# Kernel tuning notes

Measured on AMD Instinct MI355X. Metric: run time of the kernel, lower is better.

The kernel has to match this reference:

```python
import jax, jax.numpy as jnp
import numpy as np

# Dimensions derived from Mamba.__init__: d_model=512 -> joint_latent=32, mamb_latent=D=640
NL, D, DIN, DS, DTR, DC = 4, 640, 1280, 16, 40, 4  # n_layer, d_model, d_inner, d_state, dt_rank, d_conv
B, V = 64, 30  # batch, joint-sequence length (repeat_joint_num)


def _rms(x, w, eps=1e-5):
    return x * jax.lax.rsqrt(jnp.mean(x * x, axis=-1, keepdims=True) + eps) * w


def _mamba_block(x, in_w, conv_w, conv_b, xp_w, dt_w, dt_b, A_log, D_skip, out_w):
    # x: [B, V, D]
    u, res = jnp.split(jnp.einsum('bvd,ed->bve', x, in_w), 2, axis=-1)  # each [B,V,DIN]
    # causal depthwise conv1d over V
    xc = jnp.pad(u.transpose(0, 2, 1), ((0, 0), (0, 0), (DC - 1, 0)))  # [B,DIN,V+DC-1]
    xc = jax.lax.conv_general_dilated(xc, conv_w[:, None, :], (1,), 'VALID',
                                      feature_group_count=DIN,
                                      dimension_numbers=('NCH', 'OIH', 'NCH'))
    u = jax.nn.silu(xc.transpose(0, 2, 1) + conv_b)  # [B,V,DIN]
    # input-dependent SSM params
    dbl = jnp.einsum('bvd,ed->bve', u, xp_w)  # [B,V,DTR+2*DS]
    delta, Bm, Cm = jnp.split(dbl, [DTR, DTR + DS], axis=-1)
    delta = jax.nn.softplus(jnp.einsum('bvr,dr->bvd', delta, dt_w) + dt_b)  # [B,V,DIN]
    A = -jnp.exp(A_log)  # [DIN,DS]
    dA = jnp.exp(delta[..., None] * A)                              # [B,V,DIN,DS]
    dBu = delta[..., None] * Bm[:, :, None, :] * u[..., None]       # [B,V,DIN,DS]

    def step(h, t):
        dA_t, dBu_t, C_t = t
        h = dA_t * h + dBu_t                      # [B,DIN,DS]
        return h, jnp.einsum('bds,bs->bd', h, C_t)

    h0 = jnp.zeros((x.shape[0], DIN, DS), x.dtype)
    _, ys = jax.lax.scan(step, h0, (dA.transpose(1, 0, 2, 3),
                                    dBu.transpose(1, 0, 2, 3),
                                    Cm.transpose(1, 0, 2)))
    y = ys.transpose(1, 0, 2) + u * D_skip        # [B,V,DIN]
    return jnp.einsum('bvd,ed->bve', y * jax.nn.silu(res), out_w)


def setup_inputs() -> dict:
    key = jax.random.key(0)
    ks = jax.random.split(key, 10)
    s = 0.02
    return {
        'x': jax.random.normal(ks[0], (B, V, D), jnp.float32),
        'vs': jax.random.randint(ks[1], (B,), 0, V),
        'norm_w': jnp.ones((NL, D), jnp.float32),
        'in_proj_w': s * jax.random.normal(ks[2], (NL, 2 * DIN, D), jnp.float32),
        'conv_w': s * jax.random.normal(ks[3], (NL, DIN, DC), jnp.float32),
        'conv_b': jnp.zeros((NL, DIN), jnp.float32),
        'x_proj_w': s * jax.random.normal(ks[4], (NL, DTR + 2 * DS, DIN), jnp.float32),
        'dt_proj_w': s * jax.random.normal(ks[5], (NL, DIN, DTR), jnp.float32),
        'dt_proj_b': jnp.full((NL, DIN), -4.0, jnp.float32) + 0.1 * jax.random.normal(ks[6], (NL, DIN), jnp.float32),
        'A_log': jnp.tile(jnp.log(jnp.arange(1.0, DS + 1.0, dtype=jnp.float32)), (NL, DIN, 1)),
        'D_skip': jnp.ones((NL, DIN), jnp.float32),
        'out_proj_w': s * jax.random.normal(ks[7], (NL, D, DIN), jnp.float32),
        'norm_f_w': jnp.ones((D,), jnp.float32),
    }


def reference(x, vs, norm_w, in_proj_w, conv_w, conv_b, x_proj_w, dt_proj_w,
              dt_proj_b, A_log, D_skip, out_proj_w, norm_f_w):
    bidx = jnp.arange(x.shape[0])[:, None]
    # batch-wise circular permutation over V (circular_permute_v)
    fwd_idx = (jnp.arange(V)[None, :] + V - vs[:, None]) % V  # [B,V]
    h = x[bidx, fwd_idx]
    for i in range(NL):
        h = h + _mamba_block(_rms(h, norm_w[i]), in_proj_w[i], conv_w[i], conv_b[i],
                             x_proj_w[i], dt_proj_w[i], dt_proj_b[i], A_log[i],
                             D_skip[i], out_proj_w[i])
    h = _rms(h, norm_f_w)
    # reverse_circular_permute_v
    rev_idx = (jnp.arange(V)[None, :] + vs[:, None]) % V
    return h[bidx, rev_idx]
```

## Files before the change

### kernel.cpp

```cpp
#include <hip/hip_runtime.h>
#include <math.h>

#define NLAYER 4
#define DMODEL 640
#define DINNER 1280
#define DSTATE 16
#define DTRANK 40
#define DCONV  4
#define BATCH  64
#define SEQ    30
#define MTOK   (BATCH*SEQ)
#define NPROJ  (2*DINNER)
#define NDBL   (DTRANK+2*DSTATE)
#define NDBLP  80
#define KSEGS  8
#define KSEG   (DINNER/KSEGS)
#define DTKP   64

#define Q1 (NLAYER*NPROJ*DMODEL/4)
#define Q2 (NLAYER*DMODEL*DINNER/4)
#define Q3 (NLAYER*NDBLP*DINNER/4)
#define Q4 (NLAYER*DINNER*DTKP/4)
#define WCTOT (Q1+Q2+Q3+Q4)

typedef unsigned short u16;
typedef __bf16 bf16x8 __attribute__((ext_vector_type(8)));
typedef float  f32x4  __attribute__((ext_vector_type(4)));
typedef unsigned short u16x8 __attribute__((ext_vector_type(8)));

__device__ __forceinline__ float siluf(float x) {
    return x / (1.0f + __expf(-x));
}

__device__ __forceinline__ u16 f2bf(float f) {
    unsigned int u = __float_as_uint(f);
    u += 0x7fffu + ((u >> 16) & 1u);
    return (u16)(u >> 16);
}

__device__ __forceinline__ float bf2f(u16 b) {
    return __uint_as_float(((unsigned int)b) << 16);
}

__global__ void k_permute(const float* __restrict__ x, const int* __restrict__ vs,
                          float* __restrict__ h) {
    int idx = blockIdx.x * blockDim.x + threadIdx.x;
    if (idx >= MTOK * DMODEL) return;
    int d  = idx % DMODEL;
    int mv = idx / DMODEL;
    int v  = mv % SEQ;
    int b  = mv / SEQ;
    int src = (v + SEQ - vs[b]) % SEQ;
    h[idx] = x[(b * SEQ + src) * DMODEL + d];
}

__global__ __launch_bounds__(256)
void k_wconv(const float* __restrict__ in_w, const float* __restrict__ out_w,
             const float* __restrict__ xp_w, const float* __restrict__ dt_w,
             u16* __restrict__ wbi, u16* __restrict__ wbo,
             u16* __restrict__ wbx, u16* __restrict__ wdt) {
    int i = blockIdx.x * 256 + threadIdx.x;
    if (i < Q1) {
        int j = i * 4;
        float4 v = *(const float4*)(in_w + j);
        ushort4 o;
        o.x = f2bf(v.x); o.y = f2bf(v.y); o.z = f2bf(v.z); o.w = f2bf(v.w);
        *(ushort4*)(wbi + j) = o;
    } else if (i < Q1 + Q2) {
        int j = (i - Q1) * 4;
        float4 v = *(const float4*)(out_w + j);
        ushort4 o;
        o.x = f2bf(v.x); o.y = f2bf(v.y); o.z = f2bf(v.z); o.w = f2bf(v.w);
        *(ushort4*)(wbo + j) = o;
    } else if (i < Q1 + Q2 + Q3) {
        int j = (i - Q1 - Q2) * 4;
        int layer = j / (NDBLP * DINNER);
        int rem   = j % (NDBLP * DINNER);
        int r = rem / DINNER, c = rem % DINNER;
        ushort4 o = make_ushort4(0, 0, 0, 0);
        if (r < NDBL) {
            float4 v = *(const float4*)(xp_w + ((size_t)layer * NDBL + r) * DINNER + c);
            o.x = f2bf(v.x); o.y = f2bf(v.y); o.z = f2bf(v.z); o.w = f2bf(v.w);
        }
        *(ushort4*)(wbx + j) = o;
    } else {
        int j = (i - Q1 - Q2 - Q3) * 4;
        int ld = j / DTKP;
        int c  = j % DTKP;
        ushort4 o = make_ushort4(0, 0, 0, 0);
        if (c < DTRANK) {
            float4 v = *(const float4*)(dt_w + (size_t)ld * DTRANK + c);
            o.x = f2bf(v.x); o.y = f2bf(v.y); o.z = f2bf(v.z); o.w = f2bf(v.w);
        }
        *(ushort4*)(wdt + j) = o;
    }
}

__global__ __launch_bounds__(64)
void k_rmsnorm(const float* __restrict__ h, const float* __restrict__ w,
               u16* __restrict__ xn) {
    int m = blockIdx.x;
    int t = threadIdx.x;
    const float* row = h + (size_t)m * DMODEL;
    float2 vv[5];
    float ss = 0.f;
    #pragma unroll
    for (int i = 0; i < 5; ++i) {
        vv[i] = *(const float2*)(row + i * 128 + t * 2);
        ss += vv[i].x * vv[i].x + vv[i].y * vv[i].y;
    }
    #pragma unroll
    for (int o = 32; o > 0; o >>= 1) ss += __shfl_xor(ss, o, 64);
    float sc = rsqrtf(ss / DMODEL + 1e-5f);
    u16* outp = xn + (size_t)m * DMODEL;
    #pragma unroll
    for (int i = 0; i < 5; ++i) {
        int d = i * 128 + t * 2;
        float2 wv = *(const float2*)(w + d);
        ushort2 o;
        o.x = f2bf(vv[i].x * sc * wv.x);
        o.y = f2bf(vv[i].y * sc * wv.y);
        *(ushort2*)(outp + d) = o;
    }
}

__global__ __launch_bounds__(512)
void k_mfma512(const u16* __restrict__ A, int lda,
               const u16* __restrict__ W,
               u16* __restrict__ Cb, int N, int K) {
    __shared__ u16 As[128 * 32];
    __shared__ u16 Bs[128 * 32];
    const int t = threadIdx.x;
    const int w = t >> 6, l = t & 63;
    const int lane15 = l & 15, quad = l >> 4;
    const int wm = w >> 1, wn = w & 1;
    const int m0 = blockIdx.y * 128, n0 = blockIdx.x * 128;

    f32x4 acc[2][4];
    #pragma unroll
    for (int i = 0; i < 2; ++i)
        #pragma unroll
        for (int j = 0; j < 4; ++j)
            acc[i][j] = (f32x4){0.f, 0.f, 0.f, 0.f};

    for (int k0 = 0; k0 < K; k0 += 32) {
        __syncthreads();
        #pragma unroll
        for (int q = 0; q < 2; ++q) {
            int c = q * 512 + t;
            if (c < 512) {
                const u16* ga = A + (size_t)(m0 + (c >> 2)) * lda + k0 + (c & 3) * 8;
                __builtin_amdgcn_global_load_lds(
                    (const __attribute__((address_space(1))) void*)ga,
                    (__attribute__((address_space(3))) void*)&As[c * 8], 16, 0, 0);
            } else {
                int cb = c - 512;
                const u16* gb = W + (size_t)(n0 + (cb >> 2)) * K + k0 + (cb & 3) * 8;
                __builtin_amdgcn_global_load_lds(
                    (const __attribute__((address_space(1))) void*)gb,
                    (__attribute__((address_space(3))) void*)&Bs[cb * 8], 16, 0, 0);
            }
        }
        __syncthreads();

        bf16x8 af[2], bfrag[4];
        #pragma unroll
        for (int i = 0; i < 2; ++i)
            af[i] = *(const bf16x8*)&As[(wm * 32 + i * 16 + lane15) * 32 + quad * 8];
        #pragma unroll
        for (int j = 0; j < 4; ++j)
            bfrag[j] = *(const bf16x8*)&Bs[(wn * 64 + j * 16 + lane15) * 32 + quad * 8];
        #pragma unroll
        for (int i = 0; i < 2; ++i)
            #pragma unroll
            for (int j = 0; j < 4; ++j)
                acc[i][j] = __builtin_amdgcn_mfma_f32_16x16x32_bf16(
                    af[i], bfrag[j], acc[i][j], 0, 0, 0);
    }

    #pragma unroll
    for (int i = 0; i < 2; ++i) {
        #pragma unroll
        for (int r = 0; r < 4; ++r) {
            int row = m0 + wm * 32 + i * 16 + quad * 4 + r;
            #pragma unroll
            for (int j = 0; j < 4; ++j) {
                int col = n0 + wn * 64 + j * 16 + lane15;
                Cb[(size_t)row * N + col] = f2bf(acc[i][j][r]);
            }
        }
    }
}

__global__ __launch_bounds__(256)
void k_mfma64(const u16* __restrict__ A, int lda,
              const u16* __restrict__ W,
              const float* __restrict__ resid,
              float* __restrict__ C, int N, int K) {
    __shared__ u16 As[64 * 32];
    __shared__ u16 Bs[64 * 32];
    const int t = threadIdx.x;
    const int w = t >> 6, l = t & 63;
    const int lane15 = l & 15, quad = l >> 4;
    const int wm = w >> 1, wn = w & 1;
    const int m0 = blockIdx.y * 64, n0 = blockIdx.x * 64;

    f32x4 acc[2][2];
    #pragma unroll
    for (int i = 0; i < 2; ++i)
        #pragma unroll
        for (int j = 0; j < 2; ++j)
            acc[i][j] = (f32x4){0.f, 0.f, 0.f, 0.f};

    for (int k0 = 0; k0 < K; k0 += 32) {
        __syncthreads();
        {
            int c = t;
            const u16* ga = A + (size_t)(m0 + (c >> 2)) * lda + k0 + (c & 3) * 8;
            __builtin_amdgcn_global_load_lds(
                (const __attribute__((address_space(1))) void*)ga,
                (__attribute__((address_space(3))) void*)&As[c * 8], 16, 0, 0);
            const u16* gb = W + (size_t)(n0 + (c >> 2)) * K + k0 + (c & 3) * 8;
            __builtin_amdgcn_global_load_lds(
                (const __attribute__((address_space(1))) void*)gb,
                (__attribute__((address_space(3))) void*)&Bs[c * 8], 16, 0, 0);
        }
        __syncthreads();

        bf16x8 af[2], bfrag[2];
        #pragma unroll
        for (int i = 0; i < 2; ++i)
            af[i] = *(const bf16x8*)&As[(wm * 32 + i * 16 + lane15) * 32 + quad * 8];
        #pragma unroll
        for (int j = 0; j < 2; ++j)
            bfrag[j] = *(const bf16x8*)&Bs[(wn * 32 + j * 16 + lane15) * 32 + quad * 8];
        #pragma unroll
        for (int i = 0; i < 2; ++i)
            #pragma unroll
            for (int j = 0; j < 2; ++j)
                acc[i][j] = __builtin_amdgcn_mfma_f32_16x16x32_bf16(
                    af[i], bfrag[j], acc[i][j], 0, 0, 0);
    }

    #pragma unroll
    for (int i = 0; i < 2; ++i) {
        #pragma unroll
        for (int r = 0; r < 4; ++r) {
            int row = m0 + wm * 32 + i * 16 + quad * 4 + r;
            #pragma unroll
            for (int j = 0; j < 2; ++j) {
                int col = n0 + wn * 32 + j * 16 + lane15;
                size_t idx = (size_t)row * N + col;
                float v = acc[i][j][r];
                if (resid) v += resid[idx];
                C[idx] = v;
            }
        }
    }
}

__global__ __launch_bounds__(256)
void k_conv(const u16* __restrict__ urb, const float* __restrict__ cw,
            const float* __restrict__ cb, u16* __restrict__ ubf) {
    int idx = blockIdx.x * 256 + threadIdx.x;
    int c = idx % DINNER;
    int b = idx / DINNER;
    const u16* up = urb + (size_t)(b * SEQ) * NPROJ + c;
    float xv[SEQ];
    #pragma unroll
    for (int v = 0; v < SEQ; ++v) xv[v] = bf2f(up[(size_t)v * NPROJ]);
    float w0 = cw[c * 4 + 0], w1 = cw[c * 4 + 1];
    float w2 = cw[c * 4 + 2], w3 = cw[c * 4 + 3];
    float bias = cb[c];
    u16* op = ubf + (size_t)(b * SEQ) * DINNER + c;
    float x0 = 0.f, x1 = 0.f, x2 = 0.f;
    #pragma unroll
    for (int v = 0; v < SEQ; ++v) {
        float x3 = xv[v];
        float o = bias + w0 * x0 + w1 * x1 + w2 * x2 + w3 * x3;
        op[(size_t)v * DINNER] = f2bf(siluf(o));
        x0 = x1; x1 = x2; x2 = x3;
    }
}

__global__ __launch_bounds__(256)
void k_xproj(const u16* __restrict__ ubf, const u16* __restrict__ wbx,
             float* __restrict__ dblp) {
    __shared__ u16 As[64 * 32];
    __shared__ u16 Bs[NDBLP * 32];
    const int t = threadIdx.x;
    const int w = t >> 6, l = t & 63;
    const int lane15 = l & 15, quad = l >> 4;
    const int seg = blockIdx.x;
    const int m0 = blockIdx.y * 64;
    const int kb = seg * KSEG;

    f32x4 acc[5];
    #pragma unroll
    for (int j = 0; j < 5; ++j) acc[j] = (f32x4){0.f, 0.f, 0.f, 0.f};

    for (int k0 = 0; k0 < KSEG; k0 += 32) {
        __syncthreads();
        {
            int c = t;
            const u16* ga = ubf + (size_t)(m0 + (c >> 2)) * DINNER + kb + k0 + (c & 3) * 8;
            __builtin_amdgcn_global_load_lds(
                (const __attribute__((address_space(1))) void*)ga,
                (__attribute__((address_space(3))) void*)&As[c * 8], 16, 0, 0);
            const u16* gb = wbx + (size_t)(c >> 2) * DINNER + kb + k0 + (c & 3) * 8;
            __builtin_amdgcn_global_load_lds(
                (const __attribute__((address_space(1))) void*)gb,
                (__attribute__((address_space(3))) void*)&Bs[c * 8], 16, 0, 0);
        }
        if (t < 64) {
            int c = 256 + t;
            const u16* gb = wbx + (size_t)(c >> 2) * DINNER + kb + k0 + (c & 3) * 8;
            __builtin_amdgcn_global_load_lds(
                (const __attribute__((address_space(1))) void*)gb,
                (__attribute__((address_space(3))) void*)&Bs[c * 8], 16, 0, 0);
        }
        __syncthreads();

        bf16x8 af = *(const bf16x8*)&As[(w * 16 + lane15) * 32 + quad * 8];
        #pragma unroll
        for (int j = 0; j < 5; ++j) {
            bf16x8 bfrag = *(const bf16x8*)&Bs[(j * 16 + lane15) * 32 + quad * 8];
            acc[j] = __builtin_amdgcn_mfma_f32_16x16x32_bf16(af, bfrag, acc[j], 0, 0, 0);
        }
    }

    float* outp = dblp + (size_t)seg * MTOK * NDBLP;
    #pragma unroll
    for (int r = 0; r < 4; ++r) {
        int row = m0 + w * 16 + quad * 4 + r;
        #pragma unroll
        for (int j = 0; j < 5; ++j) {
            int col = j * 16 + lane15;
            outp[(size_t)row * NDBLP + col] = acc[j][r];
        }
    }
}

__global__ __launch_bounds__(256)
void k_dtgemm(const float* __restrict__ dblp, const u16* __restrict__ dtwb,
              const float* __restrict__ dtb, u16* __restrict__ delta) {
    __shared__ u16 As[64 * 32];
    __shared__ u16 Bs[64 * 32];
    const int t = threadIdx.x;
    const int w = t >> 6, l = t & 63;
    const int lane15 = l & 15, quad = l >> 4;
    const int wm = w >> 1, wn = w & 1;
    const int m0 = blockIdx.y * 64, n0 = blockIdx.x * 64;
    const int row = t >> 2, koff = (t & 3) * 8;
    const int m = m0 + row;

    f32x4 acc[2][2];
    #pragma unroll
    for (int i = 0; i < 2; ++i)
        #pragma unroll
        for (int j = 0; j < 2; ++j)
            acc[i][j] = (f32x4){0.f, 0.f, 0.f, 0.f};

    #pragma unroll
    for (int k0 = 0; k0 < DTKP; k0 += 32) {
        float sums[8] = {0.f, 0.f, 0.f, 0.f, 0.f, 0.f, 0.f, 0.f};
        #pragma unroll
        for (int q = 0; q < 2; ++q) {
            int col = k0 + koff + q * 4;
            if (col < DTRANK) {
                #pragma unroll
                for (int sg = 0; sg < KSEGS; ++sg) {
                    float4 p = *(const float4*)&dblp[(size_t)sg * MTOK * NDBLP
                                                     + (size_t)m * NDBLP + col];
                    sums[q * 4 + 0] += p.x; sums[q * 4 + 1] += p.y;
                    sums[q * 4 + 2] += p.z; sums[q * 4 + 3] += p.w;
                }
            }
        }
        u16x8 av;
        #pragma unroll
        for (int e = 0; e < 8; ++e) av[e] = f2bf(sums[e]);
        __syncthreads();
        *(u16x8*)&As[row * 32 + koff] = av;
        {
            int c = t;
            const u16* gb = dtwb + (size_t)(n0 + (c >> 2)) * DTKP + k0 + (c & 3) * 8;
            __builtin_amdgcn_global_load_lds(
                (const __attribute__((address_space(1))) void*)gb,
                (__attribute__((address_space(3))) void*)&Bs[c * 8], 16, 0, 0);
        }
        __syncthreads();

        bf16x8 af[2], bfrag[2];
        #pragma unroll
        for (int i = 0; i < 2; ++i)
            af[i] = *(const bf16x8*)&As[(wm * 32 + i * 16 + lane15) * 32 + quad * 8];
        #pragma unroll
        for (int j = 0; j < 2; ++j)
            bfrag[j] = *(const bf16x8*)&Bs[(wn * 32 + j * 16 + lane15) * 32 + quad * 8];
        #pragma unroll
        for (int i = 0; i < 2; ++i)
            #pragma unroll
            for (int j = 0; j < 2; ++j)
                acc[i][j] = __builtin_amdgcn_mfma_f32_16x16x32_bf16(
                    af[i], bfrag[j], acc[i][j], 0, 0, 0);
    }

    #pragma unroll
    for (int i = 0; i < 2; ++i) {
        #pragma unroll
        for (int r = 0; r < 4; ++r) {
            int orow = m0 + wm * 32 + i * 16 + quad * 4 + r;
            #pragma unroll
            for (int j = 0; j < 2; ++j) {
                int col = n0 + wn * 32 + j * 16 + lane15;
                float vv = acc[i][j][r] + dtb[col];
                vv = (vv > 20.f) ? vv : log1pf(__expf(vv));
                delta[(size_t)orow * DINNER + col] = f2bf(vv);
            }
        }
    }
}

__global__ __launch_bounds__(256)
void k_scan(const u16* __restrict__ ubf, const u16* __restrict__ urb,
            const float* __restrict__ dblp, const u16* __restrict__ delta,
            const float* __restrict__ A_log, const float* __restrict__ Dsk,
            u16* __restrict__ y) {
    __shared__ float BC[SEQ][2 * DSTATE];
    const int b  = blockIdx.x / (DINNER / 256);
    const int dc = blockIdx.x % (DINNER / 256);
    const int d  = dc * 256 + threadIdx.x;

    for (int t = threadIdx.x; t < SEQ * 2 * DSTATE; t += 256) {
        int v = t >> 5, s = t & 31;
        float acc = 0.f;
        #pragma unroll
        for (int sg = 0; sg < KSEGS; ++sg)
            acc += dblp[(size_t)sg * MTOK * NDBLP + (size_t)(b * SEQ + v) * NDBLP + DTRANK + s];
        BC[v][s] = acc;
    }
    __syncthreads();

    float dl[SEQ], uu[SEQ], rr[SEQ];
    #pragma unroll
    for (int v = 0; v < SEQ; ++v)
        dl[v] = bf2f(delta[(size_t)(b * SEQ + v) * DINNER + d]);
    #pragma unroll
    for (int v = 0; v < SEQ; ++v)
        uu[v] = bf2f(ubf[(size_t)(b * SEQ + v) * DINNER + d]);
    #pragma unroll
    for (int v = 0; v < SEQ; ++v)
        rr[v] = bf2f(urb[(size_t)(b * SEQ + v) * NPROJ + DINNER + d]);

    float Ar[DSTATE];
    #pragma unroll
    for (int s = 0; s < DSTATE; ++s) Ar[s] = -__expf(A_log[(size_t)d * DSTATE + s]);
    float dsk = Dsk[d];
    float st[DSTATE];
    #pragma unroll
    for (int s = 0; s < DSTATE; ++s) st[s] = 0.f;

    u16* yp = y + (size_t)(b * SEQ) * DINNER + d;

    #pragma unroll
    for (int v = 0; v < SEQ; ++v) {
        float dlt = dl[v];
        float du  = dlt * uu[v];
        float ya0 = 0.f, ya1 = 0.f, ya2 = 0.f, ya3 = 0.f;
        #pragma unroll
        for (int s = 0; s < DSTATE; s += 4) {
            float dA0 = __expf(dlt * Ar[s + 0]);
            float dA1 = __expf(dlt * Ar[s + 1]);
            float dA2 = __expf(dlt * Ar[s + 2]);
            float dA3 = __expf(dlt * Ar[s + 3]);
            st[s + 0] = dA0 * st[s + 0] + du * BC[v][s + 0];
            st[s + 1] = dA1 * st[s + 1] + du * BC[v][s + 1];
            st[s + 2] = dA2 * st[s + 2] + du * BC[v][s + 2];
            st[s + 3] = dA3 * st[s + 3] + du * BC[v][s + 3];
            ya0 += st[s + 0] * BC[v][DSTATE + s + 0];
            ya1 += st[s + 1] * BC[v][DSTATE + s + 1];
            ya2 += st[s + 2] * BC[v][DSTATE + s + 2];
            ya3 += st[s + 3] * BC[v][DSTATE + s + 3];
        }
        float ya = (ya0 + ya1) + (ya2 + ya3);
        yp[(size_t)v * DINNER] = f2bf((ya + uu[v] * dsk) * siluf(rr[v]));
    }
}

__global__ __launch_bounds__(64)
void k_final(const float* __restrict__ h, const int* __restrict__ vs,
             const float* __restrict__ w, float* __restrict__ out) {
    int mv = blockIdx.x;
    int v = mv % SEQ, b = mv / SEQ;
    int src = (v + vs[b]) % SEQ;
    const float* row = h + (size_t)(b * SEQ + src) * DMODEL;
    int t = threadIdx.x;
    float ss = 0.f;
    for (int d = t; d < DMODEL; d += 64) { float x = row[d]; ss += x * x; }
    #pragma unroll
    for (int o = 32; o > 0; o >>= 1) ss += __shfl_xor(ss, o, 64);
    float sc = rsqrtf(ss / DMODEL + 1e-5f);
    float* op = out + (size_t)mv * DMODEL;
    for (int d = t; d < DMODEL; d += 64) op[d] = row[d] * sc * w[d];
}

extern "C" void kernel_launch(void* const* d_in, const int* in_sizes, int n_in,
                              void* d_out, int out_size, void* d_ws, size_t ws_size,
                              hipStream_t stream) {
    const float* x      = (const float*)d_in[0];
    const int*   vs     = (const int*)d_in[1];
    const float* norm_w = (const float*)d_in[2];
    const float* in_w   = (const float*)d_in[3];
    const float* conv_w = (const float*)d_in[4];
    const float* conv_b = (const float*)d_in[5];
    const float* xp_w   = (const float*)d_in[6];
    const float* dt_w   = (const float*)d_in[7];
    const float* dt_b   = (const float*)d_in[8];
    const float* A_log  = (const float*)d_in[9];
    const float* Dsk    = (const float*)d_in[10];
    const float* out_w  = (const float*)d_in[11];
    const float* nfw    = (const float*)d_in[12];
    float* out = (float*)d_out;

    char* p = (char*)d_ws;
    float* h      = (float*)p; p += (size_t)MTOK * DMODEL * 4;
    u16*   xn     = (u16*)p;   p += (size_t)MTOK * DMODEL * 2;
    u16*   urb    = (u16*)p;   p += (size_t)MTOK * NPROJ * 2;
    u16*   ubf    = (u16*)p;   p += (size_t)MTOK * DINNER * 2;
    float* dblp   = (float*)p; p += (size_t)KSEGS * MTOK * NDBLP * 4;
    u16*   deltab = (u16*)p;   p += (size_t)MTOK * DINNER * 2;
    u16*   y      = (u16*)p;   p += (size_t)MTOK * DINNER * 2;
    u16*   wbi4   = (u16*)p;   p += (size_t)NLAYER * NPROJ * DMODEL * 2;
    u16*   wbo4   = (u16*)p;   p += (size_t)NLAYER * DMODEL * DINNER * 2;
    u16*   wbx4   = (u16*)p;   p += (size_t)NLAYER * NDBLP * DINNER * 2;
    u16*   wdt4   = (u16*)p;   p += (size_t)NLAYER * DINNER * DTKP * 2;

    k_wconv<<<WCTOT / 256, 256, 0, stream>>>(
        in_w, out_w, xp_w, dt_w, wbi4, wbo4, wbx4, wdt4);

    k_permute<<<(MTOK * DMODEL + 255) / 256, 256, 0, stream>>>(x, vs, h);

    for (int l = 0; l < NLAYER; ++l) {
        k_rmsnorm<<<MTOK, 64, 0, stream>>>(h, norm_w + (size_t)l * DMODEL, xn);

        k_mfma512<<<dim3(NPROJ / 128, MTOK / 128), 512, 0, stream>>>(
            xn, DMODEL, wbi4 + (size_t)l * NPROJ * DMODEL, urb, NPROJ, DMODEL);

        k_conv<<<BATCH * DINNER / 256, 256, 0, stream>>>(
            urb, conv_w + (size_t)l * DINNER * DCONV, conv_b + (size_t)l * DINNER, ubf);

        k_xproj<<<dim3(KSEGS, MTOK / 64), 256, 0, stream>>>(
            ubf, wbx4 + (size_t)l * NDBLP * DINNER, dblp);

        k_dtgemm<<<dim3(DINNER / 64, MTOK / 64), 256, 0, stream>>>(
            dblp, wdt4 + (size_t)l * DINNER * DTKP,
            dt_b + (size_t)l * DINNER, deltab);

        k_scan<<<BATCH * (DINNER / 256), 256, 0, stream>>>(
            ubf, urb, dblp, deltab,
            A_log + (size_t)l * DINNER * DSTATE, Dsk + (size_t)l * DINNER, y);

        k_mfma64<<<dim3(DMODEL / 64, MTOK / 64), 256, 0, stream>>>(
            y, DINNER, wbo4 + (size_t)l * DMODEL * DINNER, h, h, DMODEL, DINNER);
    }

    k_final<<<MTOK, 64, 0, stream>>>(h, vs, nfw, out);
}
```

Measured before the change: 504.0 us.

## Double-buffer GEMM LDS tiles with BK=64 and XOR swizzle

```diff
diff --git a/kernel.cpp b/kernel.cpp
--- a/kernel.cpp
+++ b/kernel.cpp
@@ -128,8 +128,8 @@
 void k_mfma512(const u16* __restrict__ A, int lda,
                const u16* __restrict__ W,
                u16* __restrict__ Cb, int N, int K) {
-    __shared__ u16 As[128 * 32];
-    __shared__ u16 Bs[128 * 32];
+    __shared__ u16 As[2][128 * 64];
+    __shared__ u16 Bs[2][128 * 64];
     const int t = threadIdx.x;
     const int w = t >> 6, l = t & 63;
     const int lane15 = l & 15, quad = l >> 4;
@@ -143,40 +143,57 @@
         for (int j = 0; j < 4; ++j)
             acc[i][j] = (f32x4){0.f, 0.f, 0.f, 0.f};
 
-    for (int k0 = 0; k0 < K; k0 += 32) {
+    auto stage = [&](int buf, int k0) {
+        #pragma unroll
+        for (int q = 0; q < 2; ++q) {
+            int c   = q * 512 + t;
+            int row = c >> 3;
+            int gch = ((c & 7) ^ (row & 7)) * 8;
+            const u16* ga = A + (size_t)(m0 + row) * lda + k0 + gch;
+            __builtin_amdgcn_global_load_lds(
+                (const __attribute__((address_space(1))) void*)ga,
+                (__attribute__((address_space(3))) void*)&As[buf][c * 8], 16, 0, 0);
+            const u16* gb = W + (size_t)(n0 + row) * K + k0 + gch;
+            __builtin_amdgcn_global_load_lds(
+                (const __attribute__((address_space(1))) void*)gb,
+                (__attribute__((address_space(3))) void*)&Bs[buf][c * 8], 16, 0, 0);
+        }
+    };
+
+    auto compute = [&](int buf) {
+        #pragma unroll
+        for (int ks = 0; ks < 2; ++ks) {
+            bf16x8 af[2], bfr[4];
+            #pragma unroll
+            for (int i = 0; i < 2; ++i) {
+                int row = wm * 32 + i * 16 + lane15;
+                af[i] = *(const bf16x8*)&As[buf][row * 64 + (((ks * 4 + quad) ^ (row & 7)) * 8)];
+            }
+            #pragma unroll
+            for (int j = 0; j < 4; ++j) {
+                int row = wn * 64 + j * 16 + lane15;
+                bfr[j] = *(const bf16x8*)&Bs[buf][row * 64 + (((ks * 4 + quad) ^ (row & 7)) * 8)];
+            }
+            #pragma unroll
+            for (int i = 0; i < 2; ++i)
+                #pragma unroll
+                for (int j = 0; j < 4; ++j)
+                    acc[i][j] = __builtin_amdgcn_mfma_f32_16x16x32_bf16(
+                        af[i], bfr[j], acc[i][j], 0, 0, 0);
+        }
+    };
+
+    const int NT = K >> 6;
+    stage(0, 0);
+    __syncthreads();
+    int cur = 0;
+    for (int tt = 1; tt < NT; ++tt) {
+        stage(cur ^ 1, tt * 64);
+        compute(cur);
         __syncthreads();
-        #pragma unroll
-        for (int q = 0; q < 2; ++q) {
-            int c = q * 512 + t;
-            if (c < 512) {
-                const u16* ga = A + (size_t)(m0 + (c >> 2)) * lda + k0 + (c & 3) * 8;
-                __builtin_amdgcn_global_load_lds(
-                    (const __attribute__((address_space(1))) void*)ga,
-                    (__attribute__((address_space(3))) void*)&As[c * 8], 16, 0, 0);
-            } else {
-                int cb = c - 512;
-                const u16* gb = W + (size_t)(n0 + (cb >> 2)) * K + k0 + (cb & 3) * 8;
-                __builtin_amdgcn_global_load_lds(
-                    (const __attribute__((address_space(1))) void*)gb,
-                    (__attribute__((address_space(3))) void*)&Bs[cb * 8], 16, 0, 0);
-            }
-        }
-        __syncthreads();
-
-        bf16x8 af[2], bfrag[4];
-        #pragma unroll
-        for (int i = 0; i < 2; ++i)
-            af[i] = *(const bf16x8*)&As[(wm * 32 + i * 16 + lane15) * 32 + quad * 8];
-        #pragma unroll
-        for (int j = 0; j < 4; ++j)
-            bfrag[j] = *(const bf16x8*)&Bs[(wn * 64 + j * 16 + lane15) * 32 + quad * 8];
-        #pragma unroll
-        for (int i = 0; i < 2; ++i)
-            #pragma unroll
-            for (int j = 0; j < 4; ++j)
-                acc[i][j] = __builtin_amdgcn_mfma_f32_16x16x32_bf16(
-                    af[i], bfrag[j], acc[i][j], 0, 0, 0);
-    }
+        cur ^= 1;
+    }
+    compute(cur);
 
     #pragma unroll
     for (int i = 0; i < 2; ++i) {
@@ -197,8 +214,8 @@
               const u16* __restrict__ W,
               const float* __restrict__ resid,
               float* __restrict__ C, int N, int K) {
-    __shared__ u16 As[64 * 32];
-    __shared__ u16 Bs[64 * 32];
+    __shared__ u16 As[2][64 * 64];
+    __shared__ u16 Bs[2][64 * 64];
     const int t = threadIdx.x;
     const int w = t >> 6, l = t & 63;
     const int lane15 = l & 15, quad = l >> 4;
@@ -212,35 +229,57 @@
         for (int j = 0; j < 2; ++j)
             acc[i][j] = (f32x4){0.f, 0.f, 0.f, 0.f};
 
-    for (int k0 = 0; k0 < K; k0 += 32) {
+    auto stage = [&](int buf, int k0) {
+        #pragma unroll
+        for (int q = 0; q < 2; ++q) {
+            int c   = q * 256 + t;
+            int row = c >> 3;
+            int gch = ((c & 7) ^ (row & 7)) * 8;
+            const u16* ga = A + (size_t)(m0 + row) * lda + k0 + gch;
+            __builtin_amdgcn_global_load_lds(
+                (const __attribute__((address_space(1))) void*)ga,
+                (__attribute__((address_space(3))) void*)&As[buf][c * 8], 16, 0, 0);
+            const u16* gb = W + (size_t)(n0 + row) * K + k0 + gch;
+            __builtin_amdgcn_global_load_lds(
+                (const __attribute__((address_space(1))) void*)gb,
+                (__attribute__((address_space(3))) void*)&Bs[buf][c * 8], 16, 0, 0);
+        }
+    };
+
+    auto compute = [&](int buf) {
+        #pragma unroll
+        for (int ks = 0; ks < 2; ++ks) {
+            bf16x8 af[2], bfr[2];
+            #pragma unroll
+            for (int i = 0; i < 2; ++i) {
+                int row = wm * 32 + i * 16 + lane15;
+                af[i] = *(const bf16x8*)&As[buf][row * 64 + (((ks * 4 + quad) ^ (row & 7)) * 8)];
+            }
+            #pragma unroll
+            for (int j = 0; j < 2; ++j) {
+                int row = wn * 32 + j * 16 + lane15;
+                bfr[j] = *(const bf16x8*)&Bs[buf][row * 64 + (((ks * 4 + quad) ^ (row & 7)) * 8)];
+            }
+            #pragma unroll
+            for (int i = 0; i < 2; ++i)
+                #pragma unroll
+                for (int j = 0; j < 2; ++j)
+                    acc[i][j] = __builtin_amdgcn_mfma_f32_16x16x32_bf16(
+                        af[i], bfr[j], acc[i][j], 0, 0, 0);
+        }
+    };
+
+    const int NT = K >> 6;
+    stage(0, 0);
+    __syncthreads();
+    int cur = 0;
+    for (int tt = 1; tt < NT; ++tt) {
+        stage(cur ^ 1, tt * 64);
+        compute(cur);
         __syncthreads();
-        {
-            int c = t;
-            const u16* ga = A + (size_t)(m0 + (c >> 2)) * lda + k0 + (c & 3) * 8;
-            __builtin_amdgcn_global_load_lds(
-                (const __attribute__((address_space(1))) void*)ga,
-                (__attribute__((address_space(3))) void*)&As[c * 8], 16, 0, 0);
-            const u16* gb = W + (size_t)(n0 + (c >> 2)) * K + k0 + (c & 3) * 8;
-            __builtin_amdgcn_global_load_lds(
-                (const __attribute__((address_space(1))) void*)gb,
-                (__attribute__((address_space(3))) void*)&Bs[c * 8], 16, 0, 0);
-        }
-        __syncthreads();
-
-        bf16x8 af[2], bfrag[2];
-        #pragma unroll
-        for (int i = 0; i < 2; ++i)
-            af[i] = *(const bf16x8*)&As[(wm * 32 + i * 16 + lane15) * 32 + quad * 8];
-        #pragma unroll
-        for (int j = 0; j < 2; ++j)
-            bfrag[j] = *(const bf16x8*)&Bs[(wn * 32 + j * 16 + lane15) * 32 + quad * 8];
-        #pragma unroll
-        for (int i = 0; i < 2; ++i)
-            #pragma unroll
-            for (int j = 0; j < 2; ++j)
-                acc[i][j] = __builtin_amdgcn_mfma_f32_16x16x32_bf16(
-                    af[i], bfrag[j], acc[i][j], 0, 0, 0);
-    }
+        cur ^= 1;
+    }
+    compute(cur);
 
     #pragma unroll
     for (int i = 0; i < 2; ++i) {
```

Result: faster. 466.3 us (-7.5%).
